# Kernel optimization log

Hardware: AMD Instinct MI355X
Metric: run time of the kernel (lower is better)

## Reference

```python
import jax, jax.numpy as jnp
import numpy as np

# Static config (KITTI PointPillars-style)
B, PB, N = 4, 12000, 32          # batches, pillars per batch, max points per pillar
P = B * PB
NX, NY, NZ, F = 432, 496, 1, 64  # grid and PFN output channels
PX, PY, PZ = 0.16, 0.16, 4.0     # pillar size
XO, YO, ZO = 0.08, -39.6, -1.0   # pillar-center offsets = size/2 + range_min
EPS = 1e-3                        # BatchNorm eps


def setup_inputs() -> dict:
    key = jax.random.key(0)
    ks = jax.random.split(key, 10)
    pillars = jax.random.normal(ks[0], (P, N, 8), jnp.float32)
    # unique BEV cells per batch so the scatter (torch advanced-index assign) is well-defined
    rng = np.random.default_rng(0)
    cs = []
    for b in range(B):
        lin = rng.choice(NY * NX, size=PB, replace=False)
        cs.append(np.stack([np.full(PB, b), np.zeros(PB, np.int64), lin // NX, lin % NX], 1))
    coords = jnp.asarray(np.concatenate(cs, 0), jnp.int32)  # [P,4] = (batch, z, y, x)
    num_points = jax.random.randint(ks[1], (P,), 1, N + 1, jnp.int32)

    def bn_stats(k, f):  # rows: gamma, beta, running_mean, running_var
        k1, k2, k3, k4 = jax.random.split(k, 4)
        return jnp.stack([jax.random.uniform(k1, (f,), jnp.float32, 0.8, 1.2),
                          jax.random.normal(k2, (f,)) * 0.1,
                          jax.random.normal(k3, (f,)) * 0.1,
                          jax.random.uniform(k4, (f,), jnp.float32, 0.5, 1.5)])

    return {
        'pillars': pillars,
        'w1': jax.random.normal(ks[2], (10, F), jnp.float32) * 0.1,
        'bn1': bn_stats(ks[4], F),
        'w2': jax.random.normal(ks[3], (8, F), jnp.float32) * 0.1,
        'bn2': bn_stats(ks[5], F),
        'wf1': jax.random.normal(ks[6], (F,), jnp.float32) * 0.1,
        'wf2': jax.random.normal(ks[7], (F,), jnp.float32) * 0.1,
        'fbn1': bn_stats(ks[8], 1)[:, 0],
        'fbn2': bn_stats(ks[9], 1)[:, 0],
        'coords': coords,
        'num_points': num_points,
    }


def _bn(x, stats):  # x [..., F], stats [4, F] or [4]
    g, b, m, v = stats[0], stats[1], stats[2], stats[3]
    return (x - m) * (g * jax.lax.rsqrt(v + EPS)) + b


def _pfn(x, w, stats):  # x [P, N, C] -> [P, F]: linear + BN(eval) + relu + max over points
    h = jnp.einsum('pnc,cf->pnf', x, w)
    return jax.nn.relu(_bn(h, stats)).max(axis=1)


def _forward(pillars, w1, bn1, w2, bn2, wf1, wf2, fbn1, fbn2, coords, num_points):
    xyz = pillars[:, :, :3]                                   # [P, N, 3]
    # relative xyz to cluster mean
    mean_xyz = xyz.sum(axis=1, keepdims=True) / num_points.astype(jnp.float32)[:, None, None]
    to_cluster = xyz - mean_xyz
    # relative xyz to pillar center; coords cols = (batch, z, y, x)
    cf = coords.astype(jnp.float32)
    center = jnp.stack([cf[:, 3] * PX + XO, cf[:, 2] * PY + YO, cf[:, 1] * PZ + ZO], axis=-1)
    to_center = xyz - center[:, None, :]

    pv_in = jnp.concatenate([pillars[:, :, :4], to_cluster, to_center], axis=-1)  # [P, N, 10]
    f1 = _pfn(pv_in, w1, bn1)      # [P, F] geometric stream
    f2 = _pfn(pillars, w2, bn2)    # [P, F] seg stream (full 8 channels)

    # scatter pillar features to BEV canvas: idx = z + y*nx + x (nz=1 -> z=0)
    lin = coords[:, 1] + coords[:, 2] * NX + coords[:, 3]
    b_idx = coords[:, 0]
    bev1 = jnp.zeros((B, NZ * NY * NX, F), jnp.float32).at[b_idx, lin].set(f1)
    bev2 = jnp.zeros((B, NZ * NY * NX, F), jnp.float32).at[b_idx, lin].set(f2)
    x1 = bev1.reshape(B, NY, NX, F).transpose(0, 3, 1, 2)  # [B, F, NY, NX]
    x2 = bev2.reshape(B, NY, NX, F).transpose(0, 3, 1, 2)

    # attentional fusion: 1x1 conv (no bias) + BN2d(1) per stream, softmax over the 2 weights
    s1 = _bn(jnp.einsum('bfyx,f->byx', x1, wf1), fbn1)
    s2 = _bn(jnp.einsum('bfyx,f->byx', x2, wf2), fbn2)
    aw = jax.nn.softmax(jnp.stack([s1, s2], axis=1), axis=1)  # [B, 2, NY, NX]
    return x1 * aw[:, 0:1] + x2 * aw[:, 1:2]


def reference(pillars, w1, bn1, w2, bn2, wf1, wf2, fbn1, fbn2, coords, num_points):
    return _forward(pillars, w1, bn1, w2, bn2, wf1, wf2, fbn1, fbn2, coords, num_points)
```

## Files before the change

kernel.cpp:

```cpp
#include <hip/hip_runtime.h>
#include <math.h>

#define NXC 432
#define NYC 496
#define CELLS (NYC * NXC)
#define BATCH 4
#define PTOT 48000
#define EPSC 1e-3f
#define TCELLS 128

typedef float f2v    __attribute__((ext_vector_type(2)));
typedef float f4v    __attribute__((ext_vector_type(4)));
typedef float f32x16 __attribute__((ext_vector_type(16)));
typedef __bf16 bf16x8 __attribute__((ext_vector_type(8)));
typedef unsigned int u32x2 __attribute__((ext_vector_type(2)));
typedef unsigned int u32x4 __attribute__((ext_vector_type(4)));

__device__ __forceinline__ unsigned int pk_bf16(float a, float b) {
    __bf16 ha = (__bf16)a, hb = (__bf16)b;
    unsigned short ua = __builtin_bit_cast(unsigned short, ha);
    unsigned short ub = __builtin_bit_cast(unsigned short, hb);
    return ((unsigned int)ub << 16) | ua;
}

__global__ __launch_bounds__(64) void fold_kernel(
    const float* __restrict__ w1, const float* __restrict__ bn1,
    const float* __restrict__ w2, const float* __restrict__ bn2,
    const float* __restrict__ wf1, const float* __restrict__ wf2,
    unsigned int* __restrict__ tbl)
{
    const int c = threadIdx.x;
    const float s1 = bn1[c] * rsqrtf(bn1[192 + c] + EPSC);
    const float w10 = w1[c],       w11 = w1[64 + c],  w12 = w1[128 + c];
    const float w13 = w1[192 + c], w14 = w1[256 + c], w15 = w1[320 + c];
    const float w16 = w1[384 + c], w17 = w1[448 + c], w18 = w1[512 + c];
    const float w19 = w1[576 + c];
    const float AX = (w10 + w14 + w17) * s1;
    const float AY = (w11 + w15 + w18) * s1;
    const float AZ = (w12 + w16 + w19) * s1;
    const float AI = w13 * s1;

    const float s2 = bn2[c] * rsqrtf(bn2[192 + c] + EPSC);
    float B[8];
#pragma unroll
    for (int k = 0; k < 8; ++k) B[k] = w2[k * 64 + c] * s2;

    ((u32x2*)tbl)[c]         = (u32x2){pk_bf16(AX, AY), pk_bf16(AZ, AI)};
    ((u32x4*)(tbl + 128))[c] = (u32x4){pk_bf16(B[0], B[1]), pk_bf16(B[2], B[3]),
                                       pk_bf16(B[4], B[5]), pk_bf16(B[6], B[7])};
    ((f4v*)(tbl + 384))[c]   = (f4v){bn1[64 + c] - bn1[128 + c] * s1,
                                     w14 * s1, w15 * s1, w16 * s1};
    ((f4v*)(tbl + 640))[c]   = (f4v){w17 * s1, w18 * s1, w19 * s1,
                                     bn2[64 + c] - bn2[128 + c] * s2};
    ((f2v*)(tbl + 896))[c]   = (f2v){wf1[c], wf2[c]};
}

__device__ __forceinline__ float rmax16(const f32x16 d) {
    const float t0 = fmaxf(fmaxf(d[0], d[1]), d[2]);
    const float t1 = fmaxf(fmaxf(d[3], d[4]), d[5]);
    const float t2 = fmaxf(fmaxf(d[6], d[7]), d[8]);
    const float t3 = fmaxf(fmaxf(d[9], d[10]), d[11]);
    const float t4 = fmaxf(fmaxf(d[12], d[13]), d[14]);
    const float u0 = fmaxf(fmaxf(t0, t1), t2);
    const float u1 = fmaxf(fmaxf(t3, t4), d[15]);
    return fmaxf(u0, u1);
}

__global__ __launch_bounds__(256) void pfe_kernel(
    const float* __restrict__ pillars, const unsigned int* __restrict__ tbl,
    const float* __restrict__ fbn1, const float* __restrict__ fbn2,
    const int* __restrict__ coords, const int* __restrict__ num_points,
    float* __restrict__ comb, int* __restrict__ map)
{
    const int tid  = threadIdx.x;
    const int lane = tid & 63;
    const int ln   = lane & 31;
    const bool hi  = lane >= 32;
    const int p = __builtin_amdgcn_readfirstlane(blockIdx.x * 4 + (tid >> 6));

    const u32x2* At = (const u32x2*)tbl;
    const u32x4* Bt = (const u32x4*)(tbl + 128);
    const f4v*   Ct = (const f4v*)(tbl + 384);
    const f4v*   Dt = (const f4v*)(tbl + 640);
    const f2v*   Et = (const f2v*)(tbl + 896);

    bf16x8 bfr1[2], bfr2[2];
    f4v k0c[2], k1c[2];
    f2v wfc[2];
#pragma unroll
    for (int j = 0; j < 2; ++j) {
        const int c = ln + j * 32;
        const u32x2 a2 = At[c];
        const u32x4 w1v = {a2.x, a2.y, 0u, 0u};
        bfr1[j] = __builtin_bit_cast(bf16x8, w1v);
        bfr2[j] = __builtin_bit_cast(bf16x8, Bt[c]);
        k0c[j] = Ct[c];
        k1c[j] = Dt[c];
        wfc[j] = Et[c];
    }
    const float r1s = fbn1[0] * rsqrtf(fbn1[3] + EPSC);
    const float r1b = fbn1[1], r1m = fbn1[2];
    const float r2s = fbn2[0] * rsqrtf(fbn2[3] + EPSC);
    const float r2b = fbn2[1], r2m = fbn2[2];

    const float* pl = pillars + (size_t)p * 256;
    const f4v v0 = *(const f4v*)(pl + ln * 8);
    const f4v v1 = *(const f4v*)(pl + ln * 8 + 4);
    const int cb  = coords[p * 4 + 0];
    const int cc1 = coords[p * 4 + 1];
    const int cc2 = coords[p * 4 + 2];
    const int cc3 = coords[p * 4 + 3];
    const float invn = 1.0f / (float)num_points[p];

    float sx = v0.x, sy = v0.y, sz = v0.z;
#pragma unroll
    for (int off = 1; off <= 16; off <<= 1) {
        sx += __shfl_xor(sx, off);
        sy += __shfl_xor(sy, off);
        sz += __shfl_xor(sz, off);
    }
    const float mxm = sx * invn, mym = sy * invn, mzm = sz * invn;
    const float cx = cc3 * 0.16f + 0.08f;
    const float cy = cc2 * 0.16f + (-39.6f);
    const float cz = cc1 * 4.0f  + (-1.0f);

    float C0c[2];
#pragma unroll
    for (int j = 0; j < 2; ++j)
        C0c[j] = k0c[j].x - (mxm * k0c[j].y + mym * k0c[j].z + mzm * k0c[j].w)
               - (cx * k1c[j].x + cy * k1c[j].y + cz * k1c[j].z);

    bf16x8 a;
    {
        const float f[8] = {v0.x, v0.y, v0.z, v0.w, v1.x, v1.y, v1.z, v1.w};
#pragma unroll
        for (int e = 0; e < 8; ++e) {
            const __bf16 h8 = (__bf16)f[e];
            const __bf16 l8 = (__bf16)(f[e] - (float)h8);
            a[e] = hi ? l8 : h8;
        }
    }

    const f32x16 zero = {};
    const f32x16 d0 = __builtin_amdgcn_mfma_f32_32x32x16_bf16(a, bfr1[0], zero, 0, 0, 0);
    const f32x16 d1 = __builtin_amdgcn_mfma_f32_32x32x16_bf16(a, bfr1[1], zero, 0, 0, 0);
    const f32x16 d2 = __builtin_amdgcn_mfma_f32_32x32x16_bf16(a, bfr2[0], zero, 0, 0, 0);
    const f32x16 d3 = __builtin_amdgcn_mfma_f32_32x32x16_bf16(a, bfr2[1], zero, 0, 0, 0);

    float m0 = rmax16(d0), m1 = rmax16(d1), m2 = rmax16(d2), m3 = rmax16(d3);
    m0 = fmaxf(m0, __shfl_xor(m0, 32));
    m1 = fmaxf(m1, __shfl_xor(m1, 32));
    m2 = fmaxf(m2, __shfl_xor(m2, 32));
    m3 = fmaxf(m3, __shfl_xor(m3, 32));

    const float f1A = fmaxf(m0 + C0c[0], 0.f);
    const float f1B = fmaxf(m1 + C0c[1], 0.f);
    const float f2A = fmaxf(m2 + k1c[0].w, 0.f);
    const float f2B = fmaxf(m3 + k1c[1].w, 0.f);

    float dd1 = f1A * wfc[0].x + f1B * wfc[1].x;
    float dd2 = f2A * wfc[0].y + f2B * wfc[1].y;
#pragma unroll
    for (int off = 1; off <= 16; off <<= 1) {
        dd1 += __shfl_xor(dd1, off);
        dd2 += __shfl_xor(dd2, off);
    }
    const float sc1 = (dd1 - r1m) * r1s + r1b;
    const float sc2 = (dd2 - r2m) * r2s + r2b;
    const float a0 = 1.0f / (1.0f + expf(sc2 - sc1));

    if (!hi) {
        comb[p * 64 + ln]      = fmaf(f1A - f2A, a0, f2A);
        comb[p * 64 + 32 + ln] = fmaf(f1B - f2B, a0, f2B);
    }
    if (lane == 0) {
        const int lin = cc1 + cc2 * NXC + cc3;
        map[cb * CELLS + lin] = p;
    }
}

__global__ __launch_bounds__(256) void emit_kernel(
    const int* __restrict__ map, const float* __restrict__ comb,
    float* __restrict__ out)
{
    __shared__ float lds[64 * 132];
    __shared__ int mcell[128];
    const int t = threadIdx.x;
    const int gbase = blockIdx.x * TCELLS;

    {
        const int c = t >> 1;
        const int h = (t & 1) * 32;
        const int m = map[gbase + c];
        if ((t & 1) == 0) mcell[c] = m;
        if (m >= 0) {
            const float* src = comb + (size_t)m * 64 + h;
            float* dst = lds + h * 132 + c;
#pragma unroll
            for (int j = 0; j < 8; j++) {
                const float4 v = *(const float4*)(src + j * 4);
                dst[(j * 4 + 0) * 132] = v.x;
                dst[(j * 4 + 1) * 132] = v.y;
                dst[(j * 4 + 2) * 132] = v.z;
                dst[(j * 4 + 3) * 132] = v.w;
            }
        }
    }
    __syncthreads();

    const int b = gbase / CELLS;
    const int L = gbase - b * CELLS;
    float* obase = out + (size_t)(b * 64) * CELLS + L;
#pragma unroll
    for (int r = 0; r < 8; r++) {
        const int idx = r * 256 + t;
        const int f = idx >> 5;
        const int g = idx & 31;
        const int4 mg = *(const int4*)&mcell[g * 4];
        f4v v = {0.f, 0.f, 0.f, 0.f};
        if ((mg.x & mg.y & mg.z & mg.w) >= 0) {
            const f4v w = *(const f4v*)(lds + f * 132 + g * 4);
            v.x = (mg.x < 0) ? 0.f : w.x;
            v.y = (mg.y < 0) ? 0.f : w.y;
            v.z = (mg.z < 0) ? 0.f : w.z;
            v.w = (mg.w < 0) ? 0.f : w.w;
        }
        *(f4v*)(obase + (size_t)f * CELLS + g * 4) = v;
    }
}

extern "C" void kernel_launch(void* const* d_in, const int* in_sizes, int n_in,
                              void* d_out, int out_size, void* d_ws, size_t ws_size,
                              hipStream_t stream) {
    const float* pillars = (const float*)d_in[0];
    const float* w1      = (const float*)d_in[1];
    const float* bn1     = (const float*)d_in[2];
    const float* w2      = (const float*)d_in[3];
    const float* bn2     = (const float*)d_in[4];
    const float* wf1     = (const float*)d_in[5];
    const float* wf2     = (const float*)d_in[6];
    const float* fbn1    = (const float*)d_in[7];
    const float* fbn2    = (const float*)d_in[8];
    const int*   coords  = (const int*)d_in[9];
    const int*   nump    = (const int*)d_in[10];
    float* out = (float*)d_out;

    int*   map  = (int*)d_ws;
    float* comb = (float*)((char*)d_ws + (size_t)BATCH * CELLS * 4);
    unsigned int* tbl = (unsigned int*)((char*)d_ws + (size_t)BATCH * CELLS * 4
                                        + (size_t)PTOT * 64 * 4);

    (void)hipMemsetAsync(map, 0xFF, (size_t)BATCH * CELLS * 4, stream);
    fold_kernel<<<1, 64, 0, stream>>>(w1, bn1, w2, bn2, wf1, wf2, tbl);
    pfe_kernel<<<PTOT / 4, 256, 0, stream>>>(pillars, tbl, fbn1, fbn2,
                                             coords, nump, comb, map);
    emit_kernel<<<(BATCH * CELLS) / TCELLS, 256, 0, stream>>>(map, comb, out);
}
```

Before: 84.73 us.

## Fuse pillar feature computation into BEV emit kernel via cell-to-pillar map

A small scatter kernel now writes the cell-to-pillar map first. The emit kernel then computes each occupied cell's pillar features in place, with each wave looping over the occupied cells in its 32-cell slice and writing the results straight into LDS. This removes the intermediate comb buffer, saving its global write and later gather. The cost is uneven per-wave work, since sparse cells give some waves many pillars and others none, and the extra coefficient loads in every block that has an occupied cell.

```diff
diff --git a/kernel.cpp b/kernel.cpp
--- a/kernel.cpp
+++ b/kernel.cpp
@@ -55,6 +55,16 @@
     ((f2v*)(tbl + 896))[c]   = (f2v){wf1[c], wf2[c]};
 }
 
+__global__ __launch_bounds__(256) void scatter_kernel(
+    const int* __restrict__ coords, int* __restrict__ map)
+{
+    const int t = blockIdx.x * 256 + threadIdx.x;
+    if (t < PTOT) {
+        const int4 c = *(const int4*)(coords + t * 4);
+        map[c.x * CELLS + (c.y + c.z * NXC + c.w)] = t;
+    }
+}
+
 __device__ __forceinline__ float rmax16(const f32x16 d) {
     const float t0 = fmaxf(fmaxf(d[0], d[1]), d[2]);
     const float t1 = fmaxf(fmaxf(d[3], d[4]), d[5]);
@@ -66,143 +76,126 @@
     return fmaxf(u0, u1);
 }
 
-__global__ __launch_bounds__(256) void pfe_kernel(
+__global__ __launch_bounds__(256) void fused_kernel(
     const float* __restrict__ pillars, const unsigned int* __restrict__ tbl,
     const float* __restrict__ fbn1, const float* __restrict__ fbn2,
     const int* __restrict__ coords, const int* __restrict__ num_points,
-    float* __restrict__ comb, int* __restrict__ map)
+    const int* __restrict__ map, float* __restrict__ out)
 {
+    __shared__ float lds[64 * 132];
+    __shared__ int mcell[128];
     const int tid  = threadIdx.x;
     const int lane = tid & 63;
     const int ln   = lane & 31;
     const bool hi  = lane >= 32;
-    const int p = __builtin_amdgcn_readfirstlane(blockIdx.x * 4 + (tid >> 6));
-
-    const u32x2* At = (const u32x2*)tbl;
-    const u32x4* Bt = (const u32x4*)(tbl + 128);
-    const f4v*   Ct = (const f4v*)(tbl + 384);
-    const f4v*   Dt = (const f4v*)(tbl + 640);
-    const f2v*   Et = (const f2v*)(tbl + 896);
-
-    bf16x8 bfr1[2], bfr2[2];
-    f4v k0c[2], k1c[2];
-    f2v wfc[2];
-#pragma unroll
-    for (int j = 0; j < 2; ++j) {
-        const int c = ln + j * 32;
-        const u32x2 a2 = At[c];
-        const u32x4 w1v = {a2.x, a2.y, 0u, 0u};
-        bfr1[j] = __builtin_bit_cast(bf16x8, w1v);
-        bfr2[j] = __builtin_bit_cast(bf16x8, Bt[c]);
-        k0c[j] = Ct[c];
-        k1c[j] = Dt[c];
-        wfc[j] = Et[c];
-    }
-    const float r1s = fbn1[0] * rsqrtf(fbn1[3] + EPSC);
-    const float r1b = fbn1[1], r1m = fbn1[2];
-    const float r2s = fbn2[0] * rsqrtf(fbn2[3] + EPSC);
-    const float r2b = fbn2[1], r2m = fbn2[2];
-
-    const float* pl = pillars + (size_t)p * 256;
-    const f4v v0 = *(const f4v*)(pl + ln * 8);
-    const f4v v1 = *(const f4v*)(pl + ln * 8 + 4);
-    const int cb  = coords[p * 4 + 0];
-    const int cc1 = coords[p * 4 + 1];
-    const int cc2 = coords[p * 4 + 2];
-    const int cc3 = coords[p * 4 + 3];
-    const float invn = 1.0f / (float)num_points[p];
-
-    float sx = v0.x, sy = v0.y, sz = v0.z;
-#pragma unroll
-    for (int off = 1; off <= 16; off <<= 1) {
-        sx += __shfl_xor(sx, off);
-        sy += __shfl_xor(sy, off);
-        sz += __shfl_xor(sz, off);
-    }
-    const float mxm = sx * invn, mym = sy * invn, mzm = sz * invn;
-    const float cx = cc3 * 0.16f + 0.08f;
-    const float cy = cc2 * 0.16f + (-39.6f);
-    const float cz = cc1 * 4.0f  + (-1.0f);
-
-    float C0c[2];
-#pragma unroll
-    for (int j = 0; j < 2; ++j)
-        C0c[j] = k0c[j].x - (mxm * k0c[j].y + mym * k0c[j].z + mzm * k0c[j].w)
-               - (cx * k1c[j].x + cy * k1c[j].y + cz * k1c[j].z);
-
-    bf16x8 a;
-    {
-        const float f[8] = {v0.x, v0.y, v0.z, v0.w, v1.x, v1.y, v1.z, v1.w};
-#pragma unroll
-        for (int e = 0; e < 8; ++e) {
-            const __bf16 h8 = (__bf16)f[e];
-            const __bf16 l8 = (__bf16)(f[e] - (float)h8);
-            a[e] = hi ? l8 : h8;
+    const int w    = tid >> 6;
+    const int gbase = blockIdx.x * TCELLS;
+    const int cellbase = w * 32;
+
+    const int m = map[gbase + cellbase + ln];
+    if (!hi) mcell[cellbase + ln] = m;
+    unsigned int mask = (unsigned int)(__ballot(m >= 0) & 0xffffffffu);
+
+    if (mask) {
+        const u32x2* At = (const u32x2*)tbl;
+        const u32x4* Bt = (const u32x4*)(tbl + 128);
+        const f4v*   Ct = (const f4v*)(tbl + 384);
+        const f4v*   Dt = (const f4v*)(tbl + 640);
+        const f2v*   Et = (const f2v*)(tbl + 896);
+
+        bf16x8 bfr1[2], bfr2[2];
+        f4v k0c[2], k1c[2];
+        f2v wfc[2];
+#pragma unroll
+        for (int j = 0; j < 2; ++j) {
+            const int c = ln + j * 32;
+            const u32x2 a2 = At[c];
+            const u32x4 w1v = {a2.x, a2.y, 0u, 0u};
+            bfr1[j] = __builtin_bit_cast(bf16x8, w1v);
+            bfr2[j] = __builtin_bit_cast(bf16x8, Bt[c]);
+            k0c[j] = Ct[c];
+            k1c[j] = Dt[c];
+            wfc[j] = Et[c];
         }
-    }
-
-    const f32x16 zero = {};
-    const f32x16 d0 = __builtin_amdgcn_mfma_f32_32x32x16_bf16(a, bfr1[0], zero, 0, 0, 0);
-    const f32x16 d1 = __builtin_amdgcn_mfma_f32_32x32x16_bf16(a, bfr1[1], zero, 0, 0, 0);
-    const f32x16 d2 = __builtin_amdgcn_mfma_f32_32x32x16_bf16(a, bfr2[0], zero, 0, 0, 0);
-    const f32x16 d3 = __builtin_amdgcn_mfma_f32_32x32x16_bf16(a, bfr2[1], zero, 0, 0, 0);
-
-    float m0 = rmax16(d0), m1 = rmax16(d1), m2 = rmax16(d2), m3 = rmax16(d3);
-    m0 = fmaxf(m0, __shfl_xor(m0, 32));
-    m1 = fmaxf(m1, __shfl_xor(m1, 32));
-    m2 = fmaxf(m2, __shfl_xor(m2, 32));
-    m3 = fmaxf(m3, __shfl_xor(m3, 32));
-
-    const float f1A = fmaxf(m0 + C0c[0], 0.f);
-    const float f1B = fmaxf(m1 + C0c[1], 0.f);
-    const float f2A = fmaxf(m2 + k1c[0].w, 0.f);
-    const float f2B = fmaxf(m3 + k1c[1].w, 0.f);
-
-    float dd1 = f1A * wfc[0].x + f1B * wfc[1].x;
-    float dd2 = f2A * wfc[0].y + f2B * wfc[1].y;
-#pragma unroll
-    for (int off = 1; off <= 16; off <<= 1) {
-        dd1 += __shfl_xor(dd1, off);
-        dd2 += __shfl_xor(dd2, off);
-    }
-    const float sc1 = (dd1 - r1m) * r1s + r1b;
-    const float sc2 = (dd2 - r2m) * r2s + r2b;
-    const float a0 = 1.0f / (1.0f + expf(sc2 - sc1));
-
-    if (!hi) {
-        comb[p * 64 + ln]      = fmaf(f1A - f2A, a0, f2A);
-        comb[p * 64 + 32 + ln] = fmaf(f1B - f2B, a0, f2B);
-    }
-    if (lane == 0) {
-        const int lin = cc1 + cc2 * NXC + cc3;
-        map[cb * CELLS + lin] = p;
-    }
-}
-
-__global__ __launch_bounds__(256) void emit_kernel(
-    const int* __restrict__ map, const float* __restrict__ comb,
-    float* __restrict__ out)
-{
-    __shared__ float lds[64 * 132];
-    __shared__ int mcell[128];
-    const int t = threadIdx.x;
-    const int gbase = blockIdx.x * TCELLS;
-
-    {
-        const int c = t >> 1;
-        const int h = (t & 1) * 32;
-        const int m = map[gbase + c];
-        if ((t & 1) == 0) mcell[c] = m;
-        if (m >= 0) {
-            const float* src = comb + (size_t)m * 64 + h;
-            float* dst = lds + h * 132 + c;
-#pragma unroll
-            for (int j = 0; j < 8; j++) {
-                const float4 v = *(const float4*)(src + j * 4);
-                dst[(j * 4 + 0) * 132] = v.x;
-                dst[(j * 4 + 1) * 132] = v.y;
-                dst[(j * 4 + 2) * 132] = v.z;
-                dst[(j * 4 + 3) * 132] = v.w;
+        const float r1s = fbn1[0] * rsqrtf(fbn1[3] + EPSC);
+        const float r1b = fbn1[1], r1m = fbn1[2];
+        const float r2s = fbn2[0] * rsqrtf(fbn2[3] + EPSC);
+        const float r2b = fbn2[1], r2m = fbn2[2];
+
+        while (mask) {
+            const int i = __builtin_ctz(mask);
+            mask &= mask - 1;
+            const int p = __builtin_amdgcn_readfirstlane(__shfl(m, i));
+
+            const float* pl = pillars + (size_t)p * 256;
+            const f4v v0 = *(const f4v*)(pl + ln * 8);
+            const f4v v1 = *(const f4v*)(pl + ln * 8 + 4);
+            const int cc1 = coords[p * 4 + 1];
+            const int cc2 = coords[p * 4 + 2];
+            const int cc3 = coords[p * 4 + 3];
+            const float invn = 1.0f / (float)num_points[p];
+
+            float sx = v0.x, sy = v0.y, sz = v0.z;
+#pragma unroll
+            for (int off = 1; off <= 16; off <<= 1) {
+                sx += __shfl_xor(sx, off);
+                sy += __shfl_xor(sy, off);
+                sz += __shfl_xor(sz, off);
+            }
+            const float mxm = sx * invn, mym = sy * invn, mzm = sz * invn;
+            const float cx = cc3 * 0.16f + 0.08f;
+            const float cy = cc2 * 0.16f + (-39.6f);
+            const float cz = cc1 * 4.0f  + (-1.0f);
+
+            float C0c[2];
+#pragma unroll
+            for (int j = 0; j < 2; ++j)
+                C0c[j] = k0c[j].x - (mxm * k0c[j].y + mym * k0c[j].z + mzm * k0c[j].w)
+                       - (cx * k1c[j].x + cy * k1c[j].y + cz * k1c[j].z);
+
+            bf16x8 a;
+            {
+                const float f[8] = {v0.x, v0.y, v0.z, v0.w, v1.x, v1.y, v1.z, v1.w};
+#pragma unroll
+                for (int e = 0; e < 8; ++e) {
+                    const __bf16 h8 = (__bf16)f[e];
+                    const __bf16 l8 = (__bf16)(f[e] - (float)h8);
+                    a[e] = hi ? l8 : h8;
+                }
+            }
+
+            const f32x16 zero = {};
+            const f32x16 d0 = __builtin_amdgcn_mfma_f32_32x32x16_bf16(a, bfr1[0], zero, 0, 0, 0);
+            const f32x16 d1 = __builtin_amdgcn_mfma_f32_32x32x16_bf16(a, bfr1[1], zero, 0, 0, 0);
+            const f32x16 d2 = __builtin_amdgcn_mfma_f32_32x32x16_bf16(a, bfr2[0], zero, 0, 0, 0);
+            const f32x16 d3 = __builtin_amdgcn_mfma_f32_32x32x16_bf16(a, bfr2[1], zero, 0, 0, 0);
+
+            float m0 = rmax16(d0), m1 = rmax16(d1), m2 = rmax16(d2), m3 = rmax16(d3);
+            m0 = fmaxf(m0, __shfl_xor(m0, 32));
+            m1 = fmaxf(m1, __shfl_xor(m1, 32));
+            m2 = fmaxf(m2, __shfl_xor(m2, 32));
+            m3 = fmaxf(m3, __shfl_xor(m3, 32));
+
+            const float f1A = fmaxf(m0 + C0c[0], 0.f);
+            const float f1B = fmaxf(m1 + C0c[1], 0.f);
+            const float f2A = fmaxf(m2 + k1c[0].w, 0.f);
+            const float f2B = fmaxf(m3 + k1c[1].w, 0.f);
+
+            float dd1 = f1A * wfc[0].x + f1B * wfc[1].x;
+            float dd2 = f2A * wfc[0].y + f2B * wfc[1].y;
+#pragma unroll
+            for (int off = 1; off <= 16; off <<= 1) {
+                dd1 += __shfl_xor(dd1, off);
+                dd2 += __shfl_xor(dd2, off);
+            }
+            const float sc1 = (dd1 - r1m) * r1s + r1b;
+            const float sc2 = (dd2 - r2m) * r2s + r2b;
+            const float a0 = 1.0f / (1.0f + expf(sc2 - sc1));
+
+            if (!hi) {
+                const int cp = cellbase + i;
+                lds[ln * 132 + cp]        = fmaf(f1A - f2A, a0, f2A);
+                lds[(ln + 32) * 132 + cp] = fmaf(f1B - f2B, a0, f2B);
             }
         }
     }
@@ -213,17 +206,17 @@
     float* obase = out + (size_t)(b * 64) * CELLS + L;
 #pragma unroll
     for (int r = 0; r < 8; r++) {
-        const int idx = r * 256 + t;
+        const int idx = r * 256 + tid;
         const int f = idx >> 5;
         const int g = idx & 31;
         const int4 mg = *(const int4*)&mcell[g * 4];
         f4v v = {0.f, 0.f, 0.f, 0.f};
         if ((mg.x & mg.y & mg.z & mg.w) >= 0) {
-            const f4v w = *(const f4v*)(lds + f * 132 + g * 4);
-            v.x = (mg.x < 0) ? 0.f : w.x;
-            v.y = (mg.y < 0) ? 0.f : w.y;
-            v.z = (mg.z < 0) ? 0.f : w.z;
-            v.w = (mg.w < 0) ? 0.f : w.w;
+            const f4v ww = *(const f4v*)(lds + f * 132 + g * 4);
+            v.x = (mg.x < 0) ? 0.f : ww.x;
+            v.y = (mg.y < 0) ? 0.f : ww.y;
+            v.z = (mg.z < 0) ? 0.f : ww.z;
+            v.w = (mg.w < 0) ? 0.f : ww.w;
         }
         *(f4v*)(obase + (size_t)f * CELLS + g * 4) = v;
     }
@@ -246,13 +239,11 @@
     float* out = (float*)d_out;
 
     int*   map  = (int*)d_ws;
-    float* comb = (float*)((char*)d_ws + (size_t)BATCH * CELLS * 4);
-    unsigned int* tbl = (unsigned int*)((char*)d_ws + (size_t)BATCH * CELLS * 4
-                                        + (size_t)PTOT * 64 * 4);
+    unsigned int* tbl = (unsigned int*)((char*)d_ws + (size_t)BATCH * CELLS * 4);
 
     (void)hipMemsetAsync(map, 0xFF, (size_t)BATCH * CELLS * 4, stream);
     fold_kernel<<<1, 64, 0, stream>>>(w1, bn1, w2, bn2, wf1, wf2, tbl);
-    pfe_kernel<<<PTOT / 4, 256, 0, stream>>>(pillars, tbl, fbn1, fbn2,
-                                             coords, nump, comb, map);
-    emit_kernel<<<(BATCH * CELLS) / TCELLS, 256, 0, stream>>>(map, comb, out);
-}
+    scatter_kernel<<<(PTOT + 255) / 256, 256, 0, stream>>>(coords, map);
+    fused_kernel<<<(BATCH * CELLS) / TCELLS, 256, 0, stream>>>(
+        pillars, tbl, fbn1, fbn2, coords, nump, map, out);
+}
```

Result: slower. 92.03 us (+8.6%).
